# Kernel tuning notes

Measured on AMD Instinct MI355X. Metric: run time of the kernel, lower is better.

The kernel has to match this reference:

```python
import jax, jax.numpy as jnp
import numpy as np

B, P, O, C = 64, 8732, 32, 81
IMG = 224.0
THRESH = 0.5
NEG_POS = 3.0
ALPHA = 1.0


def cxcy_to_xy(b):
    return jnp.concatenate([b[..., :2] - b[..., 2:] / 2, b[..., :2] + b[..., 2:] / 2], -1)


def xy_to_cxcy(b):
    return jnp.concatenate([(b[..., :2] + b[..., 2:]) / 2, b[..., 2:] - b[..., :2]], -1)


def coco_to_xy(b):  # [x, y, w, h] -> [xmin, ymin, xmax, ymax]
    return jnp.concatenate([b[..., :2], b[..., :2] + b[..., 2:]], -1)


def cxcy_to_gcxgcy(cxcy, priors):  # SSD offset encoding, variances 10 / 5
    g_cxcy = (cxcy[..., :2] - priors[..., :2]) / (priors[..., 2:] / 10.0)
    g_wh = jnp.log(cxcy[..., 2:] / priors[..., 2:]) * 5.0
    return jnp.concatenate([g_cxcy, g_wh], -1)


def pairwise_iou(a, b):  # a: [O,4] xy, b: [P,4] xy -> [O,P]
    lt = jnp.maximum(a[:, None, :2], b[None, :, :2])
    rb = jnp.minimum(a[:, None, 2:], b[None, :, 2:])
    wh = jnp.clip(rb - lt, 0.0)
    inter = wh[..., 0] * wh[..., 1]
    area_a = (a[:, 2] - a[:, 0]) * (a[:, 3] - a[:, 1])
    area_b = (b[:, 2] - b[:, 0]) * (b[:, 3] - b[:, 1])
    return inter / (area_a[:, None] + area_b[None, :] - inter)


def setup_inputs() -> dict:
    key = jax.random.key(0)
    k1, k2, k3, k4, k5, k6, k7 = jax.random.split(key, 7)
    pred_locs = jax.random.normal(k1, (B, P, 4), dtype=jnp.float32)
    pred_scores = jax.random.normal(k2, (B, P, C), dtype=jnp.float32)
    # COCO-format gt boxes [x, y, w, h] in pixel coords, guaranteed inside image
    xy = jax.random.uniform(k3, (B, O, 2), minval=0.0, maxval=IMG * 0.55)
    wh = jax.random.uniform(k4, (B, O, 2), minval=8.0, maxval=IMG * 0.4)
    gt_boxes = jnp.concatenate([xy, wh], -1)
    gt_labels = jax.random.randint(k5, (B, O), 1, C)  # foreground labels 1..C-1
    p_cxcy = jax.random.uniform(k6, (P, 2), minval=0.05, maxval=0.95)
    p_wh = jax.random.uniform(k7, (P, 2), minval=0.05, maxval=0.5)
    priors_cxcy = jnp.concatenate([p_cxcy, p_wh], -1)
    return {"pred_locs": pred_locs, "pred_scores": pred_scores,
            "gt_boxes": gt_boxes, "gt_labels": gt_labels,
            "priors_cxcy": priors_cxcy}


def reference(pred_locs, pred_scores, gt_boxes, gt_labels, priors_cxcy):
    priors_xy = cxcy_to_xy(priors_cxcy)

    def match(boxes_coco, labels):  # one image: [O,4] coco, [O] int
        boxes_xy = coco_to_xy(boxes_coco) / IMG  # normalize to [0,1]
        ov = pairwise_iou(boxes_xy, priors_xy)  # [O, P]
        overlap_for_prior = ov.max(axis=0)       # [P]
        object_for_prior = ov.argmax(axis=0)     # [P]
        prior_for_object = ov.argmax(axis=1)     # [O]
        # force each object to claim its best prior
        object_for_prior = object_for_prior.at[prior_for_object].set(jnp.arange(O))
        overlap_for_prior = overlap_for_prior.at[prior_for_object].set(1.0)
        label_for_prior = labels[object_for_prior]
        label_for_prior = jnp.where(overlap_for_prior < THRESH, 0, label_for_prior)
        true_locs = cxcy_to_gcxgcy(xy_to_cxcy(boxes_xy[object_for_prior]), priors_cxcy)
        return true_locs, label_for_prior

    true_locs, true_classes = jax.vmap(match)(gt_boxes, gt_labels)  # [B,P,4], [B,P]

    positive = true_classes != 0          # [B, P]
    n_pos = positive.sum(axis=1)          # [B]
    n_pos_cl = jnp.maximum(n_pos, 1).astype(jnp.float32)
    n_hard_neg = NEG_POS * n_pos_cl

    # SmoothL1 (beta=1), mean over positive prior coords
    diff = jnp.abs(pred_locs - true_locs)
    sl1 = jnp.where(diff < 1.0, 0.5 * diff * diff, diff - 0.5)  # [B,P,4]
    total_pos = n_pos.sum()
    loc_loss = jnp.where(
        total_pos > 0,
        jnp.where(positive[..., None], sl1, 0.0).sum()
        / jnp.maximum(total_pos * 4, 1).astype(jnp.float32),
        0.0,
    )

    # per-prior cross entropy
    logp = jax.nn.log_softmax(pred_scores, axis=-1)
    ce = -jnp.take_along_axis(logp, true_classes[..., None], axis=-1)[..., 0]  # [B,P]

    conf_pos_sum = jnp.where(positive, ce, 0.0).sum()
    ce_neg = jnp.where(positive, 0.0, ce)
    ce_neg_sorted = -jnp.sort(-ce_neg, axis=1)  # descending per image
    ranks = jnp.arange(P)[None, :]
    hard = ranks < n_hard_neg[:, None]
    conf_hard_neg_sum = jnp.where(hard, ce_neg_sorted, 0.0).sum()

    conf_loss = (conf_hard_neg_sum + conf_pos_sum) / n_pos_cl.sum()
    return conf_loss + ALPHA * loc_loss
```

## Files before the change

kernel.cpp:

```cpp
#include <hip/hip_runtime.h>
#include <cstdint>
#include <cstddef>

#define BB 64
#define PP 8732
#define OO 32
#define CC 81
#define NR 64
#define NB3 137

__global__ __launch_bounds__(1024) void k_prep(
    const float* __restrict__ gt_boxes,
    const float4* __restrict__ priors,
    int* __restrict__ pfo,
    int* __restrict__ done)
{
    int b = blockIdx.x, t = threadIdx.x;
    if (b == 0 && t == 0) *done = 0;
    int o = t >> 5, s = t & 31;
    __shared__ float4 s_pr[1024];
    const float* g = gt_boxes + ((size_t)b * OO + o) * 4;
    float x1 = g[0] / 224.0f, y1 = g[1] / 224.0f;
    float x2 = (g[0] + g[2]) / 224.0f, y2 = (g[1] + g[3]) / 224.0f;
    float area = (x2 - x1) * (y2 - y1);
    float best = -1.0f; int bp = 0;
    for (int base = 0; base < PP; base += 1024) {
        int idx = base + t;
        if (idx < PP) s_pr[t] = priors[idx];
        __syncthreads();
        int lim = PP - base; if (lim > 1024) lim = 1024;
        for (int j = s; j < lim; j += 32) {
            float4 pr = s_pr[j];
            float px1 = pr.x - pr.z * 0.5f, py1 = pr.y - pr.w * 0.5f;
            float px2 = pr.x + pr.z * 0.5f, py2 = pr.y + pr.w * 0.5f;
            float parea = (px2 - px1) * (py2 - py1);
            float lx = fmaxf(x1, px1), ly = fmaxf(y1, py1);
            float rx = fminf(x2, px2), ry = fminf(y2, py2);
            float w = fmaxf(rx - lx, 0.0f), h = fmaxf(ry - ly, 0.0f);
            float inter = w * h;
            float iou = inter / (area + parea - inter);
            if (iou > best) { best = iou; bp = base + j; }
        }
        __syncthreads();
    }
    unsigned long long v = ((unsigned long long)__float_as_uint(best) << 32)
                         | (unsigned long long)(0xFFFFFFFFu - (unsigned)bp);
    #pragma unroll
    for (int sh = 16; sh >= 1; sh >>= 1) {
        unsigned long long u = __shfl_xor(v, sh, 32);
        if (u > v) v = u;
    }
    if (s == 0) pfo[b * OO + o] = (int)(0xFFFFFFFFu - (unsigned)(v & 0xFFFFFFFFull));
}

__global__ __launch_bounds__(256) void k_ce(
    const float* __restrict__ scores,
    const float4* __restrict__ pred_locs,
    const float* __restrict__ gt_boxes,
    const int* __restrict__ gt_labels,
    const float4* __restrict__ priors,
    const int* __restrict__ pfo,
    float* __restrict__ ceneg,
    float* __restrict__ pp_posce, float* __restrict__ pp_sl1,
    int* __restrict__ pp_np)
{
    int b = blockIdx.y, tid = threadIdx.x;
    int row0 = blockIdx.x * NR;
    int nrows = PP - row0; if (nrows > NR) nrows = NR;

    __shared__ float sv[NR * CC];
    __shared__ float4 s_pr[NR];
    __shared__ float bx1[OO], by1[OO], bx2[OO], by2[OO], bar[OO];
    __shared__ int s_lab[OO];
    __shared__ int s_force[NR];
    __shared__ float s_cn[NR];
    __shared__ float s_posce, s_sl1;
    __shared__ int s_np;

    if (tid == 0) { s_posce = 0.f; s_sl1 = 0.f; s_np = 0; }
    if (tid < OO) {
        const float* g = gt_boxes + ((size_t)b * OO + tid) * 4;
        float x1 = g[0] / 224.0f, y1 = g[1] / 224.0f;
        float x2 = (g[0] + g[2]) / 224.0f, y2 = (g[1] + g[3]) / 224.0f;
        bx1[tid] = x1; by1[tid] = y1; bx2[tid] = x2; by2[tid] = y2;
        bar[tid] = (x2 - x1) * (y2 - y1);
        s_lab[tid] = gt_labels[b * OO + tid];
    }
    if (tid < NR) {
        s_force[tid] = -1;
        if (row0 + tid < PP) s_pr[tid] = priors[row0 + tid];
    }
    __syncthreads();
    if (tid == 0) {
        #pragma unroll
        for (int o = 0; o < OO; ++o) {
            int rp = pfo[b * OO + o] - row0;
            if (rp >= 0 && rp < nrows) s_force[rp] = o;
        }
    }
    {
        const float4* src4 = (const float4*)(scores + ((size_t)b * PP + row0) * CC);
        int nvec = nrows * CC / 4;
        float4* dst = (float4*)sv;
        for (int i = tid; i < nvec; i += 256) dst[i] = src4[i];
    }
    __syncthreads();

    int g = tid >> 4, lane = tid & 15;
    #pragma unroll
    for (int j = 0; j < 4; ++j) {
        int r = g + 16 * j;
        if (r < nrows) {
            float4 pq = s_pr[r];
            float px1 = pq.x - pq.z * 0.5f, py1 = pq.y - pq.w * 0.5f;
            float px2 = pq.x + pq.z * 0.5f, py2 = pq.y + pq.w * 0.5f;
            float parea = (px2 - px1) * (py2 - py1);
            float bi; int bo;
            {
                int o1 = lane, o2 = lane + 16;
                float lx = fmaxf(bx1[o1], px1), ly = fmaxf(by1[o1], py1);
                float rx = fminf(bx2[o1], px2), ry = fminf(by2[o1], py2);
                float w1 = fmaxf(rx - lx, 0.0f), h1 = fmaxf(ry - ly, 0.0f);
                float in1 = w1 * h1;
                float i1 = in1 / (bar[o1] + parea - in1);
                lx = fmaxf(bx1[o2], px1); ly = fmaxf(by1[o2], py1);
                rx = fminf(bx2[o2], px2); ry = fminf(by2[o2], py2);
                float w2 = fmaxf(rx - lx, 0.0f), h2 = fmaxf(ry - ly, 0.0f);
                float in2 = w2 * h2;
                float i2 = in2 / (bar[o2] + parea - in2);
                bi = i1; bo = o1;
                if (i2 > bi) { bi = i2; bo = o2; }
                unsigned long long pk = ((unsigned long long)__float_as_uint(bi) << 32)
                                      | (unsigned long long)(0xFFFFFFFFu - (unsigned)bo);
                #pragma unroll
                for (int s = 8; s >= 1; s >>= 1) {
                    unsigned long long u = __shfl_xor(pk, s, 16);
                    if (u > pk) pk = u;
                }
                bi = __uint_as_float((unsigned)(pk >> 32));
                bo = (int)(0xFFFFFFFFu - (unsigned)(pk & 0xFFFFFFFFull));
            }
            int fo = s_force[r];
            int lab, ob;
            if (fo >= 0) { ob = fo; lab = s_lab[fo]; }
            else         { ob = bo; lab = (bi < 0.5f) ? 0 : s_lab[bo]; }
            float se = 0.f, xl = 0.f;
            #pragma unroll
            for (int k = 0; k < 6; ++k) {
                int c = lane + 16 * k;
                if (c < CC) {
                    float vv = sv[r * CC + c];
                    se += __expf(vv);
                    if (c == lab) xl = vv;
                }
            }
            #pragma unroll
            for (int s = 8; s >= 1; s >>= 1) {
                se += __shfl_xor(se, s, 16);
                xl += __shfl_xor(xl, s, 16);
            }
            if (lane == 0) {
                float ce = fmaxf(__logf(se) - xl, 0.0f);
                float cn = ce;
                if (lab != 0) {
                    cn = 0.f;
                    float4 pl = pred_locs[(size_t)b * PP + row0 + r];
                    float x1 = bx1[ob], y1 = by1[ob], x2 = bx2[ob], y2 = by2[ob];
                    float cx = (x1 + x2) * 0.5f, cy = (y1 + y2) * 0.5f;
                    float w = x2 - x1, h = y2 - y1;
                    float tx = (cx - pq.x) / (pq.z / 10.0f);
                    float ty = (cy - pq.y) / (pq.w / 10.0f);
                    float tw = __logf(w / pq.z) * 5.0f;
                    float th = __logf(h / pq.w) * 5.0f;
                    float d0 = fabsf(pl.x - tx), d1 = fabsf(pl.y - ty);
                    float d2 = fabsf(pl.z - tw), d3 = fabsf(pl.w - th);
                    float sl = (d0 < 1.f ? 0.5f * d0 * d0 : d0 - 0.5f)
                             + (d1 < 1.f ? 0.5f * d1 * d1 : d1 - 0.5f)
                             + (d2 < 1.f ? 0.5f * d2 * d2 : d2 - 0.5f)
                             + (d3 < 1.f ? 0.5f * d3 * d3 : d3 - 0.5f);
                    atomicAdd(&s_posce, ce);
                    atomicAdd(&s_sl1, sl);
                    atomicAdd(&s_np, 1);
                }
                s_cn[r] = cn;
            }
        }
    }
    __syncthreads();
    if (tid < nrows) ceneg[(size_t)b * PP + row0 + tid] = s_cn[tid];
    if (tid == 0) {
        int slot = b * NB3 + blockIdx.x;
        pp_posce[slot] = s_posce;
        pp_sl1[slot]   = s_sl1;
        pp_np[slot]    = s_np;
    }
}

__global__ __launch_bounds__(512) void k_topk(
    const float* __restrict__ ceneg,
    const float* __restrict__ pp_posce, const float* __restrict__ pp_sl1,
    const int* __restrict__ pp_np,
    float* __restrict__ hard, float* __restrict__ posce_b,
    float* __restrict__ sl1_b, int* __restrict__ n_pos,
    int* __restrict__ done, float* __restrict__ out)
{
    int b = blockIdx.x, tid = threadIdx.x;
    __shared__ float4 sv4[PP / 4];
    __shared__ int hist[8][256];
    __shared__ int hsum[256];
    __shared__ int s_i[8];
    __shared__ float s_f[8], s_f2[8];
    __shared__ int s_bcast;
    __shared__ unsigned s_sel;
    __shared__ int s_krem;
    __shared__ int s_last;
    float pc = 0.f, sl = 0.f; int np = 0;
    for (int i = tid; i < NB3; i += 512) {
        pc += pp_posce[b * NB3 + i];
        sl += pp_sl1[b * NB3 + i];
        np += pp_np[b * NB3 + i];
    }
    #pragma unroll
    for (int s = 32; s >= 1; s >>= 1) {
        pc += __shfl_xor(pc, s, 64);
        sl += __shfl_xor(sl, s, 64);
        np += __shfl_xor(np, s, 64);
    }
    int wid = tid >> 6;
    if ((tid & 63) == 0) { s_i[wid] = np; s_f[wid] = pc; s_f2[wid] = sl; }
    const float4* src = (const float4*)(ceneg + (size_t)b * PP);
    for (int i = tid; i < PP / 4; i += 512) sv4[i] = src[i];
    __syncthreads();
    if (tid == 0) {
        int n = 0; float fp = 0.f, fs = 0.f;
        #pragma unroll
        for (int k = 0; k < 8; ++k) { n += s_i[k]; fp += s_f[k]; fs += s_f2[k]; }
        n_pos[b] = n; posce_b[b] = fp; sl1_b[b] = fs;
        s_bcast = n;
        int K0 = 3 * (n > 1 ? n : 1);
        if (K0 > PP) K0 = PP;
        s_sel = 0u; s_krem = K0;
    }
    __syncthreads();
    np = s_bcast;
    int K = 3 * (np > 1 ? np : 1);
    if (K > PP) K = PP;
    #pragma unroll
    for (int s = 24; s >= 0; s -= 8) {
        for (int i = tid; i < 8 * 256; i += 512) ((int*)hist)[i] = 0;
        __syncthreads();
        unsigned pref = s_sel; int krem = s_krem;
        int hs = s + 8;
        unsigned prefhi = (hs >= 32) ? 0u : (pref >> (hs & 31));
        for (int i = tid; i < PP / 4; i += 512) {
            float4 q = sv4[i];
            float vals[4] = {q.x, q.y, q.z, q.w};
            #pragma unroll
            for (int c4 = 0; c4 < 4; ++c4) {
                unsigned bts = __float_as_uint(vals[c4]);
                bool ok = (hs >= 32) || ((bts >> (hs & 31)) == prefhi);
                if (ok) atomicAdd(&hist[wid][(bts >> s) & 255], 1);
            }
        }
        __syncthreads();
        if (tid < 256) {
            int t = 0;
            #pragma unroll
            for (int k = 0; k < 8; ++k) t += hist[k][tid];
            hsum[tid] = t;
        }
        __syncthreads();
        if (tid < 64) {
            int ln = tid;
            int cum = 0;
            for (int c = 3; c >= 0; --c) {
                int h = hsum[c * 64 + ln];
                int suff = h;
                #pragma unroll
                for (int off = 1; off < 64; off <<= 1) {
                    int t = __shfl_down(suff, off);
                    if (ln + off < 64) suff += t;
                }
                int ctot = __shfl(suff, 0);
                if (cum + ctot >= krem) {
                    unsigned long long m = __ballot(cum + suff >= krem);
                    int l = 63 - __builtin_clzll(m);
                    int suffl = __shfl(suff, l);
                    int hl = __shfl(h, l);
                    if (ln == 0) {
                        s_sel = pref | ((unsigned)(c * 64 + l) << s);
                        s_krem = krem - (cum + suffl - hl);
                    }
                    break;
                }
                cum += ctot;
            }
        }
        __syncthreads();
    }
    float vk = __uint_as_float(s_sel);
    float sm = 0.f; int cg = 0;
    for (int i = tid; i < PP / 4; i += 512) {
        float4 q = sv4[i];
        if (q.x > vk) { sm += q.x; cg++; }
        if (q.y > vk) { sm += q.y; cg++; }
        if (q.z > vk) { sm += q.z; cg++; }
        if (q.w > vk) { sm += q.w; cg++; }
    }
    #pragma unroll
    for (int s = 32; s >= 1; s >>= 1) {
        sm += __shfl_xor(sm, s, 64);
        cg += __shfl_xor(cg, s, 64);
    }
    if ((tid & 63) == 0) { s_f[wid] = sm; s_i[wid] = cg; }
    __syncthreads();
    if (tid == 0) {
        float S = 0.f; int CG = 0;
        #pragma unroll
        for (int k = 0; k < 8; ++k) { S += s_f[k]; CG += s_i[k]; }
        hard[b] = S + (float)(K - CG) * vk;
    }
    __threadfence();
    if (tid == 0) s_last = (atomicAdd(done, 1) == BB - 1) ? 1 : 0;
    __syncthreads();
    if (s_last) {
        __threadfence();
        if (tid < 64) {
            int t = tid;
            int np2 = n_pos[t];
            float h2 = hard[t], pc2 = posce_b[t], sl2 = sl1_b[t];
            float cl = (float)(np2 > 1 ? np2 : 1);
            int tp = np2; float hs2 = h2; float cls = cl;
            #pragma unroll
            for (int sft = 32; sft >= 1; sft >>= 1) {
                tp  += __shfl_xor(tp, sft, 64);
                hs2 += __shfl_xor(hs2, sft, 64);
                cls += __shfl_xor(cls, sft, 64);
                pc2 += __shfl_xor(pc2, sft, 64);
                sl2 += __shfl_xor(sl2, sft, 64);
            }
            if (t == 0) {
                float conf = (hs2 + pc2) / cls;
                float loc = 0.f;
                if (tp > 0) {
                    int den = tp * 4; if (den < 1) den = 1;
                    loc = sl2 / (float)den;
                }
                out[0] = conf + loc;
            }
        }
    }
}

extern "C" void kernel_launch(void* const* d_in, const int* in_sizes, int n_in,
                              void* d_out, int out_size, void* d_ws, size_t ws_size,
                              hipStream_t stream)
{
    const float* pred_locs   = (const float*)d_in[0];
    const float* pred_scores = (const float*)d_in[1];
    const float* gt_boxes    = (const float*)d_in[2];
    const int*   gt_labels   = (const int*)d_in[3];
    const float* priors      = (const float*)d_in[4];

    char* ws = (char*)d_ws;
    const size_t npf = (size_t)BB * PP;
    size_t off = 0;
    float* ceneg = (float*)(ws + off); off += 4 * npf;
    int*   pfo   = (int*)  (ws + off); off += 4 * (size_t)BB * OO;
    float* pp_posce = (float*)(ws + off); off += 4 * (size_t)BB * NB3;
    float* pp_sl1   = (float*)(ws + off); off += 4 * (size_t)BB * NB3;
    int*   pp_np    = (int*)  (ws + off); off += 4 * (size_t)BB * NB3;
    float* posce_b  = (float*)(ws + off); off += 4 * BB;
    float* sl1_b    = (float*)(ws + off); off += 4 * BB;
    int*   n_pos    = (int*)  (ws + off); off += 4 * BB;
    float* hard     = (float*)(ws + off); off += 4 * BB;
    int*   done     = (int*)  (ws + off); off += 4;

    k_prep<<<BB, 1024, 0, stream>>>(gt_boxes, (const float4*)priors, pfo, done);

    dim3 gB(NB3, BB);
    k_ce<<<gB, 256, 0, stream>>>(pred_scores, (const float4*)pred_locs, gt_boxes, gt_labels,
                                 (const float4*)priors, pfo, ceneg,
                                 pp_posce, pp_sl1, pp_np);

    k_topk<<<BB, 512, 0, stream>>>(ceneg, pp_posce, pp_sl1, pp_np,
                                   hard, posce_b, sl1_b, n_pos, done, (float*)d_out);
}
```

Baseline: 379.0 us.

## Split prior-matching kernel across prior quarters and reduce partial maxima in CE kernel

The per-object best-prior search now launches 4 blocks per image, each scanning a quarter of the priors, instead of one block scanning all of them. Each block writes a packed (IoU, inverted index) 64-bit partial result. The CE kernel takes the max over the four partials to recover the forced prior per object, keeping the lowest-index tie-break. The inner IoU loop is also unrolled by four for more instruction-level parallelism. The aim is to fill more compute units during the matching stage, at the cost of an extra small reduction and more workspace.

```diff
diff --git a/kernel.cpp b/kernel.cpp
--- a/kernel.cpp
+++ b/kernel.cpp
@@ -8,15 +8,17 @@
 #define CC 81
 #define NR 64
 #define NB3 137
+#define NQ 4
+#define QP 2183
 
 __global__ __launch_bounds__(1024) void k_prep(
     const float* __restrict__ gt_boxes,
     const float4* __restrict__ priors,
-    int* __restrict__ pfo,
+    unsigned long long* __restrict__ part,
     int* __restrict__ done)
 {
-    int b = blockIdx.x, t = threadIdx.x;
-    if (b == 0 && t == 0) *done = 0;
+    int q = blockIdx.x, b = blockIdx.y, t = threadIdx.x;
+    if (q == 0 && b == 0 && t == 0) *done = 0;
     int o = t >> 5, s = t & 31;
     __shared__ float4 s_pr[1024];
     const float* g = gt_boxes + ((size_t)b * OO + o) * 4;
@@ -24,22 +26,33 @@
     float x2 = (g[0] + g[2]) / 224.0f, y2 = (g[1] + g[3]) / 224.0f;
     float area = (x2 - x1) * (y2 - y1);
     float best = -1.0f; int bp = 0;
-    for (int base = 0; base < PP; base += 1024) {
+    int p0 = q * QP;
+    for (int base = 0; base < QP; base += 1024) {
         int idx = base + t;
-        if (idx < PP) s_pr[t] = priors[idx];
-        __syncthreads();
-        int lim = PP - base; if (lim > 1024) lim = 1024;
-        for (int j = s; j < lim; j += 32) {
-            float4 pr = s_pr[j];
-            float px1 = pr.x - pr.z * 0.5f, py1 = pr.y - pr.w * 0.5f;
-            float px2 = pr.x + pr.z * 0.5f, py2 = pr.y + pr.w * 0.5f;
-            float parea = (px2 - px1) * (py2 - py1);
-            float lx = fmaxf(x1, px1), ly = fmaxf(y1, py1);
-            float rx = fminf(x2, px2), ry = fminf(y2, py2);
-            float w = fmaxf(rx - lx, 0.0f), h = fmaxf(ry - ly, 0.0f);
-            float inter = w * h;
-            float iou = inter / (area + parea - inter);
-            if (iou > best) { best = iou; bp = base + j; }
+        if (idx < QP) s_pr[t] = priors[p0 + idx];
+        __syncthreads();
+        int lim = QP - base; if (lim > 1024) lim = 1024;
+        for (int j = s; j < lim; j += 128) {
+            float iou4[4]; int jj4[4];
+            #pragma unroll
+            for (int u = 0; u < 4; ++u) {
+                int jj = j + 32 * u;
+                jj4[u] = jj;
+                if (jj < lim) {
+                    float4 pr = s_pr[jj];
+                    float px1 = pr.x - pr.z * 0.5f, py1 = pr.y - pr.w * 0.5f;
+                    float px2 = pr.x + pr.z * 0.5f, py2 = pr.y + pr.w * 0.5f;
+                    float parea = (px2 - px1) * (py2 - py1);
+                    float lx = fmaxf(x1, px1), ly = fmaxf(y1, py1);
+                    float rx = fminf(x2, px2), ry = fminf(y2, py2);
+                    float w = fmaxf(rx - lx, 0.0f), h = fmaxf(ry - ly, 0.0f);
+                    float inter = w * h;
+                    iou4[u] = inter / (area + parea - inter);
+                } else iou4[u] = -2.0f;
+            }
+            #pragma unroll
+            for (int u = 0; u < 4; ++u)
+                if (iou4[u] > best) { best = iou4[u]; bp = p0 + base + jj4[u]; }
         }
         __syncthreads();
     }
@@ -50,7 +63,7 @@
         unsigned long long u = __shfl_xor(v, sh, 32);
         if (u > v) v = u;
     }
-    if (s == 0) pfo[b * OO + o] = (int)(0xFFFFFFFFu - (unsigned)(v & 0xFFFFFFFFull));
+    if (s == 0) part[((size_t)b * NQ + q) * OO + o] = v;
 }
 
 __global__ __launch_bounds__(256) void k_ce(
@@ -59,7 +72,7 @@
     const float* __restrict__ gt_boxes,
     const int* __restrict__ gt_labels,
     const float4* __restrict__ priors,
-    const int* __restrict__ pfo,
+    const unsigned long long* __restrict__ part,
     float* __restrict__ ceneg,
     float* __restrict__ pp_posce, float* __restrict__ pp_sl1,
     int* __restrict__ pp_np)
@@ -72,6 +85,7 @@
     __shared__ float4 s_pr[NR];
     __shared__ float bx1[OO], by1[OO], bx2[OO], by2[OO], bar[OO];
     __shared__ int s_lab[OO];
+    __shared__ int s_pfo[OO];
     __shared__ int s_force[NR];
     __shared__ float s_cn[NR];
     __shared__ float s_posce, s_sl1;
@@ -85,6 +99,14 @@
         bx1[tid] = x1; by1[tid] = y1; bx2[tid] = x2; by2[tid] = y2;
         bar[tid] = (x2 - x1) * (y2 - y1);
         s_lab[tid] = gt_labels[b * OO + tid];
+        const unsigned long long* pb = part + (size_t)b * NQ * OO + tid;
+        unsigned long long m = pb[0];
+        #pragma unroll
+        for (int qq = 1; qq < NQ; ++qq) {
+            unsigned long long v = pb[qq * OO];
+            if (v > m) m = v;
+        }
+        s_pfo[tid] = (int)(0xFFFFFFFFu - (unsigned)(m & 0xFFFFFFFFull));
     }
     if (tid < NR) {
         s_force[tid] = -1;
@@ -94,7 +116,7 @@
     if (tid == 0) {
         #pragma unroll
         for (int o = 0; o < OO; ++o) {
-            int rp = pfo[b * OO + o] - row0;
+            int rp = s_pfo[o] - row0;
             if (rp >= 0 && rp < nrows) s_force[rp] = o;
         }
     }
@@ -366,7 +388,7 @@
     const size_t npf = (size_t)BB * PP;
     size_t off = 0;
     float* ceneg = (float*)(ws + off); off += 4 * npf;
-    int*   pfo   = (int*)  (ws + off); off += 4 * (size_t)BB * OO;
+    unsigned long long* part = (unsigned long long*)(ws + off); off += 8 * (size_t)BB * NQ * OO;
     float* pp_posce = (float*)(ws + off); off += 4 * (size_t)BB * NB3;
     float* pp_sl1   = (float*)(ws + off); off += 4 * (size_t)BB * NB3;
     int*   pp_np    = (int*)  (ws + off); off += 4 * (size_t)BB * NB3;
@@ -376,11 +398,12 @@
     float* hard     = (float*)(ws + off); off += 4 * BB;
     int*   done     = (int*)  (ws + off); off += 4;
 
-    k_prep<<<BB, 1024, 0, stream>>>(gt_boxes, (const float4*)priors, pfo, done);
+    dim3 gP(NQ, BB);
+    k_prep<<<gP, 1024, 0, stream>>>(gt_boxes, (const float4*)priors, part, done);
 
     dim3 gB(NB3, BB);
     k_ce<<<gB, 256, 0, stream>>>(pred_scores, (const float4*)pred_locs, gt_boxes, gt_labels,
-                                 (const float4*)priors, pfo, ceneg,
+                                 (const float4*)priors, part, ceneg,
                                  pp_posce, pp_sl1, pp_np);
 
     k_topk<<<BB, 512, 0, stream>>>(ceneg, pp_posce, pp_sl1, pp_np,
```

Measured after the change: 339.2 us. 1.12x faster.
